# Optimization experiments

Measured on AMD Instinct MI355X. Metric: run time of the kernel, lower is better.

The kernel has to match this reference:

```python
import jax, jax.numpy as jnp
import numpy as np

B, C, H, W = 64, 1, 1024, 1024
KS, F, OUT = 16, 128, 10
L = (H // KS) * (W // KS)  # 4096 non-overlapping patch locations


def setup_inputs() -> dict:
    key = jax.random.key(0)
    k1, k2, k3, k4, k5 = jax.random.split(key, 5)
    x = jax.random.normal(k1, (B, C, H, W), dtype=jnp.float32)
    weight = jax.random.normal(k2, (F, L, C, KS, KS), dtype=jnp.float32)
    bias = jax.random.normal(k3, (F, L, C), dtype=jnp.float32)
    dec_w = jax.random.normal(k4, (OUT, F * L * C), dtype=jnp.float32) * 0.01
    dec_b = jax.random.normal(k5, (OUT,), dtype=jnp.float32)
    return {"x": x, "weight": weight, "bias": bias, "dec_w": dec_w, "dec_b": dec_b}


def reference(x, weight, bias, dec_w, dec_b):
    b, c, h, w = x.shape
    f, l, cw, kh, kw = weight.shape
    # Non-overlapping unfold (stride == kernel): [B,C,H,W] -> [B, L, C, kh, kw]
    patches = x.reshape(b, c, h // kh, kh, w // kw, kw)
    patches = patches.transpose(0, 2, 4, 1, 3, 5).reshape(b, l, c, kh, kw)
    # Locally-connected multiply-sum: out[b,f,l,c] = sum_ij patches[b,l,c,i,j] * weight[f,l,c,i,j]
    y = jnp.einsum('blcij,flcij->bflc', patches, weight) + bias
    y = jax.nn.relu(y)
    y = y.reshape(b, -1)  # [B, F*L*C], f-major like torch's view
    return y @ dec_w.T + dec_b
```

## Files before the change

kernel.cpp:

```cpp
#include <hip/hip_runtime.h>
#include <hip/hip_bf16.h>

#define B_    64
#define F_    128
#define L_    4096
#define K_    256
#define OUT_  10
#define HW_   (1024 * 1024)
#define WIMG_ 1024

typedef __attribute__((ext_vector_type(8))) short bf16x8;
typedef __attribute__((ext_vector_type(4))) float f32x4;

static __device__ __forceinline__ unsigned short f2bf(float f) {
    return __builtin_bit_cast(unsigned short, __float2bfloat16(f));
}
static __device__ __forceinline__ bf16x8 cvt8(float4 a, float4 b) {
    bf16x8 r;
    r[0] = (short)f2bf(a.x); r[1] = (short)f2bf(a.y);
    r[2] = (short)f2bf(a.z); r[3] = (short)f2bf(a.w);
    r[4] = (short)f2bf(b.x); r[5] = (short)f2bf(b.y);
    r[6] = (short)f2bf(b.z); r[7] = (short)f2bf(b.w);
    return r;
}

__global__ __launch_bounds__(256, 3)
void lcn_main(const float* __restrict__ x, const float* __restrict__ wgt,
              const float* __restrict__ bias, const float* __restrict__ dec_w,
              float* __restrict__ ws) {
    const int l  = blockIdx.x;
    const int hb = l >> 6, wb = l & 63;
    const int t  = threadIdx.x;
    const int lane = t & 63;
    const int wc   = t >> 6;
    const int ln15 = lane & 15;
    const int kg   = lane >> 4;

    __shared__ union {
        unsigned short xs[B_ * K_];
        float ysm[B_][132];
        float red[16][B_][OUT_];
    } u;

    {
        const int b  = t >> 2;
        const int j0 = (t & 3) * 4;
        const float* xp = x + (size_t)b * HW_ + (size_t)(hb * 16) * WIMG_ + wb * 16 + j0;
        float4 v[16];
        #pragma unroll
        for (int r = 0; r < 16; ++r)
            v[r] = *reinterpret_cast<const float4*>(xp + (size_t)r * WIMG_);
        const int swz = (b & 7) << 3;
        #pragma unroll
        for (int r = 0; r < 16; ++r) {
            const int k = r * 16 + j0;
            ushort4 s4 = make_ushort4(f2bf(v[r].x), f2bf(v[r].y), f2bf(v[r].z), f2bf(v[r].w));
            *reinterpret_cast<ushort4*>(&u.xs[b * K_ + (k ^ swz)]) = s4;
        }
    }
    __syncthreads();

    const float* w0p = wgt + ((size_t)(wc * 32 + ln15) * L_ + l) * K_;
    const float* w1p = w0p + (size_t)16 * L_ * K_;

    f32x4 acc[4][2];
    #pragma unroll
    for (int m = 0; m < 4; ++m)
        #pragma unroll
        for (int n = 0; n < 2; ++n)
            acc[m][n] = (f32x4){0.f, 0.f, 0.f, 0.f};

    #pragma unroll
    for (int ks = 0; ks < 8; ++ks) {
        const int kb = ks * 32 + kg * 8;
        const float4 wa0 = *reinterpret_cast<const float4*>(w0p + kb);
        const float4 wa1 = *reinterpret_cast<const float4*>(w0p + kb + 4);
        const float4 wb0 = *reinterpret_cast<const float4*>(w1p + kb);
        const float4 wb1 = *reinterpret_cast<const float4*>(w1p + kb + 4);
        const bf16x8 b0 = cvt8(wa0, wa1);
        const bf16x8 b1 = cvt8(wb0, wb1);
        bf16x8 a[4];
        #pragma unroll
        for (int m = 0; m < 4; ++m) {
            const int b = m * 16 + ln15;
            a[m] = *reinterpret_cast<const bf16x8*>(
                &u.xs[b * K_ + (kb ^ ((b & 7) << 3))]);
        }
        #pragma unroll
        for (int m = 0; m < 4; ++m) {
            acc[m][0] = __builtin_amdgcn_mfma_f32_16x16x32_bf16(a[m], b0, acc[m][0], 0, 0, 0);
            acc[m][1] = __builtin_amdgcn_mfma_f32_16x16x32_bf16(a[m], b1, acc[m][1], 0, 0, 0);
        }
    }

    float bv[2];
    #pragma unroll
    for (int n = 0; n < 2; ++n)
        bv[n] = bias[(size_t)(wc * 32 + n * 16 + ln15) * L_ + l];

    __syncthreads();

    #pragma unroll
    for (int m = 0; m < 4; ++m)
        #pragma unroll
        for (int n = 0; n < 2; ++n)
            #pragma unroll
            for (int r = 0; r < 4; ++r) {
                const int b = m * 16 + kg * 4 + r;
                const int f = wc * 32 + n * 16 + ln15;
                u.ysm[b][f] = fmaxf(acc[m][n][r] + bv[n], 0.f);
            }
    __syncthreads();

    const int tx = t & 15, ty = t >> 4;
    const int b0_ = tx * 4, f0_ = ty * 8;

    float yv[4][8];
    #pragma unroll
    for (int bi = 0; bi < 4; ++bi) {
        f32x4 p0 = *reinterpret_cast<const f32x4*>(&u.ysm[b0_ + bi][f0_]);
        f32x4 p1 = *reinterpret_cast<const f32x4*>(&u.ysm[b0_ + bi][f0_ + 4]);
        yv[bi][0] = p0.x; yv[bi][1] = p0.y; yv[bi][2] = p0.z; yv[bi][3] = p0.w;
        yv[bi][4] = p1.x; yv[bi][5] = p1.y; yv[bi][6] = p1.z; yv[bi][7] = p1.w;
    }
    __syncthreads();

    float part[4][OUT_];
    #pragma unroll
    for (int bi = 0; bi < 4; ++bi)
        #pragma unroll
        for (int o = 0; o < OUT_; ++o) part[bi][o] = 0.f;

    #pragma unroll
    for (int fj = 0; fj < 8; ++fj) {
        #pragma unroll
        for (int o = 0; o < OUT_; ++o) {
            const float dw = dec_w[(size_t)o * ((size_t)F_ * L_) + (size_t)(f0_ + fj) * L_ + l];
            #pragma unroll
            for (int bi = 0; bi < 4; ++bi)
                part[bi][o] = fmaf(yv[bi][fj], dw, part[bi][o]);
        }
    }

    #pragma unroll
    for (int bi = 0; bi < 4; ++bi)
        #pragma unroll
        for (int o = 0; o < OUT_; ++o)
            u.red[ty][b0_ + bi][o] = part[bi][o];
    __syncthreads();

    for (int idx = t; idx < B_ * OUT_; idx += 256) {
        const int b = idx / OUT_;
        const int o = idx - b * OUT_;
        float s = 0.f;
        #pragma unroll
        for (int g = 0; g < 16; ++g) s += u.red[g][b][o];
        ws[(size_t)b * ((size_t)L_ * OUT_) + (size_t)l * OUT_ + o] = s;
    }
}

__global__ __launch_bounds__(640)
void lcn_reduce(const float* __restrict__ ws, const float* __restrict__ dec_b,
                float* __restrict__ out) {
    const int b = blockIdx.x;
    const int j = threadIdx.x;
    const float* base = ws + (size_t)b * ((size_t)L_ * OUT_);

    float s = 0.f;
    #pragma unroll 8
    for (int i = 0; i < 64; ++i)
        s += base[j + i * (64 * OUT_)];

    __shared__ float lds[64 * OUT_];
    lds[j] = s;
    __syncthreads();

    if (j < OUT_) {
        float tot = dec_b[j];
        #pragma unroll
        for (int lc = 0; lc < 64; ++lc) tot += lds[lc * OUT_ + j];
        out[b * OUT_ + j] = tot;
    }
}

extern "C" void kernel_launch(void* const* d_in, const int* in_sizes, int n_in,
                              void* d_out, int out_size, void* d_ws, size_t ws_size,
                              hipStream_t stream) {
    const float* x     = (const float*)d_in[0];
    const float* wgt   = (const float*)d_in[1];
    const float* bias  = (const float*)d_in[2];
    const float* dec_w = (const float*)d_in[3];
    const float* dec_b = (const float*)d_in[4];
    float* out = (float*)d_out;
    float* wsf = (float*)d_ws;

    lcn_main<<<dim3(L_), dim3(256), 0, stream>>>(x, wgt, bias, dec_w, wsf);
    lcn_reduce<<<dim3(B_), dim3(640), 0, stream>>>(wsf, dec_b, out);
}
```

Baseline: 267.8 us.

## Double block threads to 512, halving per-thread MFMA and decoder work

Each block now runs 8 waves instead of 4. Each wave computes one 16-wide filter tile instead of two, and the decoder step splits the 10 outputs across two thread halves. The patch load is reorganized so each thread converts and stores 8 bf16 values at once. The goal is to cut register pressure and raise memory-level parallelism for the weight-streaming loads, which dominate cost. The trade-off is more threads per block and the same LDS use per block.

```diff
diff --git a/kernel.cpp b/kernel.cpp
--- a/kernel.cpp
+++ b/kernel.cpp
@@ -11,6 +11,7 @@
 
 typedef __attribute__((ext_vector_type(8))) short bf16x8;
 typedef __attribute__((ext_vector_type(4))) float f32x4;
+typedef __attribute__((ext_vector_type(8))) unsigned short u16x8;
 
 static __device__ __forceinline__ unsigned short f2bf(float f) {
     return __builtin_bit_cast(unsigned short, __float2bfloat16(f));
@@ -24,7 +25,7 @@
     return r;
 }
 
-__global__ __launch_bounds__(256, 3)
+__global__ __launch_bounds__(512, 8)
 void lcn_main(const float* __restrict__ x, const float* __restrict__ wgt,
               const float* __restrict__ bias, const float* __restrict__ dec_w,
               float* __restrict__ ws) {
@@ -43,42 +44,34 @@
     } u;
 
     {
-        const int b  = t >> 2;
-        const int j0 = (t & 3) * 4;
-        const float* xp = x + (size_t)b * HW_ + (size_t)(hb * 16) * WIMG_ + wb * 16 + j0;
-        float4 v[16];
-        #pragma unroll
-        for (int r = 0; r < 16; ++r)
-            v[r] = *reinterpret_cast<const float4*>(xp + (size_t)r * WIMG_);
+        const int b  = t >> 3;
+        const int jl = t & 7;
+        const float* xp = x + (size_t)b * HW_ + (size_t)(hb * 16) * WIMG_ + wb * 16;
         const int swz = (b & 7) << 3;
         #pragma unroll
-        for (int r = 0; r < 16; ++r) {
-            const int k = r * 16 + j0;
-            ushort4 s4 = make_ushort4(f2bf(v[r].x), f2bf(v[r].y), f2bf(v[r].z), f2bf(v[r].w));
-            *reinterpret_cast<ushort4*>(&u.xs[b * K_ + (k ^ swz)]) = s4;
+        for (int c = 0; c < 4; ++c) {
+            const int k0  = c * 64 + jl * 8;
+            const int row = k0 >> 4, col = k0 & 15;
+            float4 v0 = *reinterpret_cast<const float4*>(xp + (size_t)row * WIMG_ + col);
+            float4 v1 = *reinterpret_cast<const float4*>(xp + (size_t)row * WIMG_ + col + 4);
+            bf16x8 s8 = cvt8(v0, v1);
+            *reinterpret_cast<bf16x8*>(&u.xs[b * K_ + (k0 ^ swz)]) = s8;
         }
     }
     __syncthreads();
 
-    const float* w0p = wgt + ((size_t)(wc * 32 + ln15) * L_ + l) * K_;
-    const float* w1p = w0p + (size_t)16 * L_ * K_;
+    const float* wp = wgt + ((size_t)(wc * 16 + ln15) * L_ + l) * K_;
 
-    f32x4 acc[4][2];
+    f32x4 acc[4];
     #pragma unroll
-    for (int m = 0; m < 4; ++m)
-        #pragma unroll
-        for (int n = 0; n < 2; ++n)
-            acc[m][n] = (f32x4){0.f, 0.f, 0.f, 0.f};
+    for (int m = 0; m < 4; ++m) acc[m] = (f32x4){0.f, 0.f, 0.f, 0.f};
 
     #pragma unroll
     for (int ks = 0; ks < 8; ++ks) {
         const int kb = ks * 32 + kg * 8;
-        const float4 wa0 = *reinterpret_cast<const float4*>(w0p + kb);
-        const float4 wa1 = *reinterpret_cast<const float4*>(w0p + kb + 4);
-        const float4 wb0 = *reinterpret_cast<const float4*>(w1p + kb);
-        const float4 wb1 = *reinterpret_cast<const float4*>(w1p + kb + 4);
-        const bf16x8 b0 = cvt8(wa0, wa1);
-        const bf16x8 b1 = cvt8(wb0, wb1);
+        const float4 w0 = *reinterpret_cast<const float4*>(wp + kb);
+        const float4 w1 = *reinterpret_cast<const float4*>(wp + kb + 4);
+        const bf16x8 bw = cvt8(w0, w1);
         bf16x8 a[4];
         #pragma unroll
         for (int m = 0; m < 4; ++m) {
@@ -87,32 +80,27 @@
                 &u.xs[b * K_ + (kb ^ ((b & 7) << 3))]);
         }
         #pragma unroll
-        for (int m = 0; m < 4; ++m) {
-            acc[m][0] = __builtin_amdgcn_mfma_f32_16x16x32_bf16(a[m], b0, acc[m][0], 0, 0, 0);
-            acc[m][1] = __builtin_amdgcn_mfma_f32_16x16x32_bf16(a[m], b1, acc[m][1], 0, 0, 0);
-        }
+        for (int m = 0; m < 4; ++m)
+            acc[m] = __builtin_amdgcn_mfma_f32_16x16x32_bf16(a[m], bw, acc[m], 0, 0, 0);
     }
 
-    float bv[2];
-    #pragma unroll
-    for (int n = 0; n < 2; ++n)
-        bv[n] = bias[(size_t)(wc * 32 + n * 16 + ln15) * L_ + l];
+    const float bv = bias[(size_t)(wc * 16 + ln15) * L_ + l];
 
     __syncthreads();
 
     #pragma unroll
     for (int m = 0; m < 4; ++m)
         #pragma unroll
-        for (int n = 0; n < 2; ++n)
-            #pragma unroll
-            for (int r = 0; r < 4; ++r) {
-                const int b = m * 16 + kg * 4 + r;
-                const int f = wc * 32 + n * 16 + ln15;
-                u.ysm[b][f] = fmaxf(acc[m][n][r] + bv[n], 0.f);
-            }
+        for (int r = 0; r < 4; ++r) {
+            const int b = m * 16 + kg * 4 + r;
+            const int f = wc * 16 + ln15;
+            u.ysm[b][f] = fmaxf(acc[m][r] + bv, 0.f);
+        }
     __syncthreads();
 
-    const int tx = t & 15, ty = t >> 4;
+    const int tt = t & 255;
+    const int oh = t >> 8;
+    const int tx = tt & 15, ty = tt >> 4;
     const int b0_ = tx * 4, f0_ = ty * 8;
 
     float yv[4][8];
@@ -125,31 +113,32 @@
     }
     __syncthreads();
 
-    float part[4][OUT_];
+    float part[4][5];
     #pragma unroll
     for (int bi = 0; bi < 4; ++bi)
         #pragma unroll
-        for (int o = 0; o < OUT_; ++o) part[bi][o] = 0.f;
+        for (int oo = 0; oo < 5; ++oo) part[bi][oo] = 0.f;
 
     #pragma unroll
     for (int fj = 0; fj < 8; ++fj) {
         #pragma unroll
-        for (int o = 0; o < OUT_; ++o) {
+        for (int oo = 0; oo < 5; ++oo) {
+            const int o = oh * 5 + oo;
             const float dw = dec_w[(size_t)o * ((size_t)F_ * L_) + (size_t)(f0_ + fj) * L_ + l];
             #pragma unroll
             for (int bi = 0; bi < 4; ++bi)
-                part[bi][o] = fmaf(yv[bi][fj], dw, part[bi][o]);
+                part[bi][oo] = fmaf(yv[bi][fj], dw, part[bi][oo]);
         }
     }
 
     #pragma unroll
     for (int bi = 0; bi < 4; ++bi)
         #pragma unroll
-        for (int o = 0; o < OUT_; ++o)
-            u.red[ty][b0_ + bi][o] = part[bi][o];
+        for (int oo = 0; oo < 5; ++oo)
+            u.red[ty][b0_ + bi][oh * 5 + oo] = part[bi][oo];
     __syncthreads();
 
-    for (int idx = t; idx < B_ * OUT_; idx += 256) {
+    for (int idx = t; idx < B_ * OUT_; idx += 512) {
         const int b = idx / OUT_;
         const int o = idx - b * OUT_;
         float s = 0.f;
@@ -194,6 +183,6 @@
     float* out = (float*)d_out;
     float* wsf = (float*)d_ws;
 
-    lcn_main<<<dim3(L_), dim3(256), 0, stream>>>(x, wgt, bias, dec_w, wsf);
+    lcn_main<<<dim3(L_), dim3(512), 0, stream>>>(x, wgt, bias, dec_w, wsf);
     lcn_reduce<<<dim3(B_), dim3(640), 0, stream>>>(wsf, dec_b, out);
 }
```

New measurement: 299.2 us. +11.7%, slower.

## Stream weights through LDS in eight phases with async global_load_lds prefetch

Applied to the files above, without the earlier changes.

The main kernel now walks the 128 filters in eight phases of 16. Each phase's fp32 weight slice is loaded asynchronously into LDS with global_load_lds, prefetching the next phase while the current one is consumed. Each wave does 16 batch rows with one MFMA accumulator, and the ReLU output is staged in LDS as bf16 so the decoder dot product runs per phase, with a smaller cross-thread reduction at the end. The aim is to overlap weight streaming with compute and cut register pressure. The cost is many more block barriers, per-phase bias and dec_w loads, and bf16 rounding of the hidden activations.

```diff
diff --git a/kernel.cpp b/kernel.cpp
--- a/kernel.cpp
+++ b/kernel.cpp
@@ -8,12 +8,19 @@
 #define OUT_  10
 #define HW_   (1024 * 1024)
 #define WIMG_ 1024
+#define NPH   8
+#define WMP   260
+#define YMP   20
 
 typedef __attribute__((ext_vector_type(8))) short bf16x8;
 typedef __attribute__((ext_vector_type(4))) float f32x4;
 
 static __device__ __forceinline__ unsigned short f2bf(float f) {
     return __builtin_bit_cast(unsigned short, __float2bfloat16(f));
+}
+static __device__ __forceinline__ float bf2f(unsigned short h) {
+    unsigned int i = ((unsigned int)h) << 16;
+    return __builtin_bit_cast(float, i);
 }
 static __device__ __forceinline__ bf16x8 cvt8(float4 a, float4 b) {
     bf16x8 r;
@@ -32,130 +39,107 @@
     const int hb = l >> 6, wb = l & 63;
     const int t  = threadIdx.x;
     const int lane = t & 63;
-    const int wc   = t >> 6;
+    const int wid  = t >> 6;
     const int ln15 = lane & 15;
     const int kg   = lane >> 4;
 
     __shared__ union {
-        unsigned short xs[B_ * K_];
-        float ysm[B_][132];
-        float red[16][B_][OUT_];
+        struct {
+            unsigned short xs[B_ * K_];
+            float          wm[16 * WMP];
+            unsigned short ym[B_ * YMP];
+        } s;
+        float red[4 * B_ * OUT_];
     } u;
+
+    auto GLL = [&](int p) {
+        #pragma unroll
+        for (int i = 0; i < 4; ++i) {
+            const int fl = wid * 4 + i;
+            const float* gp = wgt + ((size_t)(p * 16 + fl) * L_ + l) * K_ + lane * 4;
+            __builtin_amdgcn_global_load_lds(
+                (const __attribute__((address_space(1))) void*)gp,
+                (__attribute__((address_space(3))) void*)&u.s.wm[fl * WMP],
+                16, 0, 0);
+        }
+    };
+    GLL(0);
 
     {
         const int b  = t >> 2;
-        const int j0 = (t & 3) * 4;
-        const float* xp = x + (size_t)b * HW_ + (size_t)(hb * 16) * WIMG_ + wb * 16 + j0;
-        float4 v[16];
-        #pragma unroll
-        for (int r = 0; r < 16; ++r)
-            v[r] = *reinterpret_cast<const float4*>(xp + (size_t)r * WIMG_);
+        const int c4 = t & 3;
+        const float* xb = x + (size_t)b * HW_ + (size_t)(hb * 16) * WIMG_
+                            + wb * 16 + c4 * 4;
         const int swz = (b & 7) << 3;
         #pragma unroll
         for (int r = 0; r < 16; ++r) {
-            const int k = r * 16 + j0;
-            ushort4 s4 = make_ushort4(f2bf(v[r].x), f2bf(v[r].y), f2bf(v[r].z), f2bf(v[r].w));
-            *reinterpret_cast<ushort4*>(&u.xs[b * K_ + (k ^ swz)]) = s4;
+            float4 v = *reinterpret_cast<const float4*>(xb + (size_t)r * WIMG_);
+            const int k = r * 16 + c4 * 4;
+            *reinterpret_cast<ushort4*>(&u.s.xs[b * K_ + (k ^ swz)]) =
+                make_ushort4(f2bf(v.x), f2bf(v.y), f2bf(v.z), f2bf(v.w));
         }
     }
     __syncthreads();
 
-    const float* w0p = wgt + ((size_t)(wc * 32 + ln15) * L_ + l) * K_;
-    const float* w1p = w0p + (size_t)16 * L_ * K_;
+    const int bl   = wid * 16 + ln15;
+    const int xswz = (bl & 7) << 3;
+    const int db   = t & 63;
+    const int fq   = t >> 6;
 
-    f32x4 acc[4][2];
+    float part[OUT_];
     #pragma unroll
-    for (int m = 0; m < 4; ++m)
+    for (int o = 0; o < OUT_; ++o) part[o] = 0.f;
+
+    for (int p = 0; p < NPH; ++p) {
+        const float bv = bias[(size_t)(p * 16 + ln15) * L_ + l];
+        f32x4 acc = (f32x4){0.f, 0.f, 0.f, 0.f};
         #pragma unroll
-        for (int n = 0; n < 2; ++n)
-            acc[m][n] = (f32x4){0.f, 0.f, 0.f, 0.f};
-
-    #pragma unroll
-    for (int ks = 0; ks < 8; ++ks) {
-        const int kb = ks * 32 + kg * 8;
-        const float4 wa0 = *reinterpret_cast<const float4*>(w0p + kb);
-        const float4 wa1 = *reinterpret_cast<const float4*>(w0p + kb + 4);
-        const float4 wb0 = *reinterpret_cast<const float4*>(w1p + kb);
-        const float4 wb1 = *reinterpret_cast<const float4*>(w1p + kb + 4);
-        const bf16x8 b0 = cvt8(wa0, wa1);
-        const bf16x8 b1 = cvt8(wb0, wb1);
-        bf16x8 a[4];
-        #pragma unroll
-        for (int m = 0; m < 4; ++m) {
-            const int b = m * 16 + ln15;
-            a[m] = *reinterpret_cast<const bf16x8*>(
-                &u.xs[b * K_ + (kb ^ ((b & 7) << 3))]);
+        for (int ks = 0; ks < 8; ++ks) {
+            const int kb = ks * 32 + kg * 8;
+            const bf16x8 a = *reinterpret_cast<const bf16x8*>(
+                &u.s.xs[bl * K_ + (kb ^ xswz)]);
+            const float* wr = &u.s.wm[ln15 * WMP + kb];
+            float4 w0 = *reinterpret_cast<const float4*>(wr);
+            float4 w1 = *reinterpret_cast<const float4*>(wr + 4);
+            const bf16x8 bw = cvt8(w0, w1);
+            acc = __builtin_amdgcn_mfma_f32_16x16x32_bf16(a, bw, acc, 0, 0, 0);
         }
         #pragma unroll
-        for (int m = 0; m < 4; ++m) {
-            acc[m][0] = __builtin_amdgcn_mfma_f32_16x16x32_bf16(a[m], b0, acc[m][0], 0, 0, 0);
-            acc[m][1] = __builtin_amdgcn_mfma_f32_16x16x32_bf16(a[m], b1, acc[m][1], 0, 0, 0);
+        for (int r = 0; r < 4; ++r) {
+            const int b = wid * 16 + kg * 4 + r;
+            u.s.ym[b * YMP + ln15] = f2bf(fmaxf(acc[r] + bv, 0.f));
         }
-    }
+        __syncthreads();
 
-    float bv[2];
-    #pragma unroll
-    for (int n = 0; n < 2; ++n)
-        bv[n] = bias[(size_t)(wc * 32 + n * 16 + ln15) * L_ + l];
+        if (p + 1 < NPH) GLL(p + 1);
 
-    __syncthreads();
-
-    #pragma unroll
-    for (int m = 0; m < 4; ++m)
-        #pragma unroll
-        for (int n = 0; n < 2; ++n)
-            #pragma unroll
-            for (int r = 0; r < 4; ++r) {
-                const int b = m * 16 + kg * 4 + r;
-                const int f = wc * 32 + n * 16 + ln15;
-                u.ysm[b][f] = fmaxf(acc[m][n][r] + bv[n], 0.f);
-            }
-    __syncthreads();
-
-    const int tx = t & 15, ty = t >> 4;
-    const int b0_ = tx * 4, f0_ = ty * 8;
-
-    float yv[4][8];
-    #pragma unroll
-    for (int bi = 0; bi < 4; ++bi) {
-        f32x4 p0 = *reinterpret_cast<const f32x4*>(&u.ysm[b0_ + bi][f0_]);
-        f32x4 p1 = *reinterpret_cast<const f32x4*>(&u.ysm[b0_ + bi][f0_ + 4]);
-        yv[bi][0] = p0.x; yv[bi][1] = p0.y; yv[bi][2] = p0.z; yv[bi][3] = p0.w;
-        yv[bi][4] = p1.x; yv[bi][5] = p1.y; yv[bi][6] = p1.z; yv[bi][7] = p1.w;
-    }
-    __syncthreads();
-
-    float part[4][OUT_];
-    #pragma unroll
-    for (int bi = 0; bi < 4; ++bi)
-        #pragma unroll
-        for (int o = 0; o < OUT_; ++o) part[bi][o] = 0.f;
-
-    #pragma unroll
-    for (int fj = 0; fj < 8; ++fj) {
+        ushort4 yb = *reinterpret_cast<const ushort4*>(&u.s.ym[db * YMP + fq * 4]);
+        const float yv0 = bf2f(yb.x), yv1 = bf2f(yb.y),
+                    yv2 = bf2f(yb.z), yv3 = bf2f(yb.w);
         #pragma unroll
         for (int o = 0; o < OUT_; ++o) {
-            const float dw = dec_w[(size_t)o * ((size_t)F_ * L_) + (size_t)(f0_ + fj) * L_ + l];
-            #pragma unroll
-            for (int bi = 0; bi < 4; ++bi)
-                part[bi][o] = fmaf(yv[bi][fj], dw, part[bi][o]);
+            const size_t dwbase = ((size_t)o * F_ + p * 16 + fq * 4) * L_ + l;
+            float s = part[o];
+            s = fmaf(yv0, dec_w[dwbase],          s);
+            s = fmaf(yv1, dec_w[dwbase + L_],     s);
+            s = fmaf(yv2, dec_w[dwbase + 2 * L_], s);
+            s = fmaf(yv3, dec_w[dwbase + 3 * L_], s);
+            part[o] = s;
         }
+        __syncthreads();
     }
 
     #pragma unroll
-    for (int bi = 0; bi < 4; ++bi)
-        #pragma unroll
-        for (int o = 0; o < OUT_; ++o)
-            u.red[ty][b0_ + bi][o] = part[bi][o];
+    for (int o = 0; o < OUT_; ++o)
+        u.red[(fq * B_ + db) * OUT_ + o] = part[o];
     __syncthreads();
 
     for (int idx = t; idx < B_ * OUT_; idx += 256) {
         const int b = idx / OUT_;
         const int o = idx - b * OUT_;
-        float s = 0.f;
-        #pragma unroll
-        for (int g = 0; g < 16; ++g) s += u.red[g][b][o];
-        ws[(size_t)b * ((size_t)L_ * OUT_) + (size_t)l * OUT_ + o] = s;
+        float s = u.red[(0 * B_ + b) * OUT_ + o] + u.red[(1 * B_ + b) * OUT_ + o]
+                + u.red[(2 * B_ + b) * OUT_ + o] + u.red[(3 * B_ + b) * OUT_ + o];
+        ws[((size_t)b * L_ + l) * OUT_ + o] = s;
     }
 }
 
@@ -171,7 +155,7 @@
     for (int i = 0; i < 64; ++i)
         s += base[j + i * (64 * OUT_)];
 
-    __shared__ float lds[64 * OUT_];
+    __shared__ float lds[640];
     lds[j] = s;
     __syncthreads();
 
```

Measured after the change: 446.6 us. 1.67x slower.
